# Performance work log

Measured on AMD Instinct MI355X. Metric: run time of the kernel, lower is better.

The kernel has to match this reference:

```python
import jax, jax.numpy as jnp
import numpy as np

DIM = 512
HEADS = 16
WIN = (7, 7)
N = WIN[0] * WIN[1]
B_ = 4096
HEAD_DIM = DIM // HEADS
SCALE = HEAD_DIM ** (-0.5)


def _relative_position_index():
    ch = np.arange(WIN[0])
    cw = np.arange(WIN[1])
    coords = np.stack(np.meshgrid(ch, cw, indexing='ij'))  # (2, Wh, Ww)
    cf = coords.reshape(2, -1)                               # (2, N)
    rel = cf[:, :, None] - cf[:, None, :]                    # (2, N, N)
    rel = rel.transpose(1, 2, 0).astype(np.int32)            # (N, N, 2)
    rel[:, :, 0] += WIN[0] - 1
    rel[:, :, 1] += WIN[1] - 1
    rel[:, :, 0] *= 2 * WIN[1] - 1
    return jnp.asarray(rel.sum(-1))                          # (N, N) int32


def setup_inputs() -> dict:
    key = jax.random.key(0)
    ks = jax.random.split(key, 6)
    x = jax.random.normal(ks[0], (B_, N, DIM), dtype=jnp.float32)
    qkv_w = jax.random.normal(ks[1], (3 * DIM, DIM), dtype=jnp.float32) * (DIM ** -0.5)
    qkv_b = jnp.zeros((3 * DIM,), dtype=jnp.float32)
    proj_w = jax.random.normal(ks[2], (DIM, DIM), dtype=jnp.float32) * (DIM ** -0.5)
    proj_b = jnp.zeros((DIM,), dtype=jnp.float32)
    n_rel = (2 * WIN[0] - 1) * (2 * WIN[1] - 1)  # 169
    bias_table = jax.random.normal(ks[3], (n_rel, HEADS), dtype=jnp.float32) * 0.02
    rel_idx = _relative_position_index()
    return {"x": x, "qkv_w": qkv_w, "qkv_b": qkv_b, "proj_w": proj_w,
            "proj_b": proj_b, "bias_table": bias_table, "rel_idx": rel_idx}


def reference(x, qkv_w, qkv_b, proj_w, proj_b, bias_table, rel_idx):
    B, n, C = x.shape
    # qkv projection: (B, N, 3C) -> (3, B, H, N, hd)
    qkv = x @ qkv_w.T + qkv_b
    qkv = qkv.reshape(B, n, 3, HEADS, HEAD_DIM).transpose(2, 0, 3, 1, 4)
    q, k, v = qkv[0], qkv[1], qkv[2]
    q = q * SCALE
    attn = jnp.einsum('bhnd,bhmd->bhnm', q, k)               # (B, H, N, N)
    # gather relative position bias: (N*N, H) -> (H, N, N)
    bias = bias_table[rel_idx.reshape(-1)].reshape(n, n, HEADS).transpose(2, 0, 1)
    attn = jax.nn.softmax(attn + bias[None], axis=-1)
    out = jnp.einsum('bhnm,bhmd->bhnd', attn, v)
    out = out.transpose(0, 2, 1, 3).reshape(B, n, C)
    return out @ proj_w.T + proj_b
```

## Files before the change

### kernel.cpp

```cpp
#include <hip/hip_runtime.h>
#include <cstdint>
#include <type_traits>

#define B_WIN 4096
#define NTOK 49
#define DIMC 512
#define HEADS 16
#define HD 32
#define M_ROWS (B_WIN * NTOK)
#define SCALE 0.17677669529663689f

using bf16x8 = __attribute__((ext_vector_type(8))) short;
using f32x4  = __attribute__((ext_vector_type(4))) float;
using u16x8  = __attribute__((ext_vector_type(8))) unsigned short;

__device__ inline unsigned short f2bf(float f) {
    uint32_t u = __float_as_uint(f);
    uint32_t r = (u + 0x7fffu + ((u >> 16) & 1u)) >> 16;
    return (unsigned short)r;
}
__device__ inline unsigned int pk2(float lo, float hi) {
    return (unsigned int)f2bf(lo) | ((unsigned int)f2bf(hi) << 16);
}

__device__ __forceinline__ void gll16(const unsigned short* g, unsigned short* l) {
    __builtin_amdgcn_global_load_lds(
        (const __attribute__((address_space(1))) void*)g,
        (__attribute__((address_space(3))) void*)l, 16, 0, 0);
}

#define DSR(dst, addr) asm volatile("ds_read_b128 %0, %1" : "=v"(dst) : "v"(addr))
#define SCHED0() __builtin_amdgcn_sched_barrier(0)
#define BARRIER() do { SCHED0(); __builtin_amdgcn_s_barrier(); SCHED0(); } while (0)
#define LGKM0() do { asm volatile("s_waitcnt lgkmcnt(0)"); SCHED0(); } while (0)

__global__ __launch_bounds__(256) void cvt_f32_bf16(
    const float* __restrict__ in, unsigned short* __restrict__ out, int n4)
{
    for (int i = blockIdx.x * blockDim.x + threadIdx.x; i < n4;
         i += gridDim.x * blockDim.x) {
        float4 v = reinterpret_cast<const float4*>(in)[i];
        ushort4 o;
        o.x = f2bf(v.x); o.y = f2bf(v.y); o.z = f2bf(v.z); o.w = f2bf(v.w);
        reinterpret_cast<ushort4*>(out)[i] = o;
    }
}

__global__ __launch_bounds__(256) void build_bias(
    const float* __restrict__ btab, const int* __restrict__ ridx,
    float* __restrict__ biasPad)
{
    const int idx = blockIdx.x * 256 + threadIdx.x;
    const int h = idx >> 12, rem = idx & 4095;
    const int i = rem >> 6, j = rem & 63;
    float v = -1e30f;
    if (i < NTOK && j < NTOK) v = btab[ridx[i * NTOK + j] * HEADS + h];
    biasPad[idx] = v;
}

template <int OUTF32>
__global__ __launch_bounds__(512, 2) void gemm8p(
    const unsigned short* __restrict__ A,
    const unsigned short* __restrict__ W,
    const float* __restrict__ bias,
    void* __restrict__ Craw,
    int N, int ntn)
{
    extern __shared__ unsigned short lds[];
    constexpr int K = 512, NT = 8;

    const int nwg = gridDim.x;
    const int bid = blockIdx.x;
    const int wg = (bid & 7) * (nwg >> 3) + (bid >> 3);
    const int tn = wg % ntn, tm = wg / ntn;
    const size_t m0 = (size_t)tm * 256, n0 = (size_t)tn * 256;

    const int t = threadIdx.x;
    const int lane = t & 63, wid = t >> 6;
    const int wm = wid >> 2, wn = wid & 3;
    const int l15 = lane & 15, l4 = lane >> 4;

    const unsigned short* pA[2];
    const unsigned short* pB[2];
    int dA[2], dB[2];
#pragma unroll
    for (int u = 0; u < 2; ++u) {
        const int f = t + u * 512, rl = f >> 3, c = f & 7, g = c ^ (rl & 7);
        const int lrA = (rl & 63) + (rl >> 6) * 128;
        const int lrB = ((rl >> 5) << 6) + (rl & 31);
        pA[u] = A + (m0 + lrA) * K + g * 8;
        pB[u] = W + (n0 + lrB) * K + g * 8;
        dA[u] = lrA * 64 + c * 8;
        dB[u] = 32768 + lrB * 64 + c * 8;
    }
#define STG_A(h, T) { const int _b = ((T) & 1) * 16384, _kt = (T) * 64;      \
    gll16(pA[0] + (h) * 64 * K + _kt, lds + _b + dA[0] + (h) * 4096);        \
    gll16(pA[1] + (h) * 64 * K + _kt, lds + _b + dA[1] + (h) * 4096); }
#define STG_B(h, T) { const int _b = ((T) & 1) * 16384, _kt = (T) * 64;      \
    gll16(pB[0] + (h) * 32 * K + _kt, lds + _b + dB[0] + (h) * 2048);        \
    gll16(pB[1] + (h) * 32 * K + _kt, lds + _b + dB[1] + (h) * 2048); }

    const unsigned lbase = (unsigned)(uintptr_t)lds;
    const unsigned swz = (unsigned)(l15 & 7);
    const unsigned cx0 = ((0u + l4) ^ swz) * 16u;
    const unsigned cx1 = ((4u + l4) ^ swz) * 16u;
    const unsigned arow = (unsigned)(wm * 128 + l15) * 128u;
    const unsigned brow = (unsigned)(wn * 64 + l15) * 128u;

    f32x4 acc[8][4] = {};
    bf16x8 a[4][2], b0[2][2], b1[2][2];

    STG_A(0, 0); STG_B(0, 0); STG_A(1, 0); STG_B(1, 0);
    STG_A(0, 1); STG_B(0, 1); STG_A(1, 1);
    asm volatile("s_waitcnt vmcnt(6)");
    SCHED0();
    BARRIER();

    for (int S = 0; S < NT; ++S) {
        const int bs = S & 1;
        const unsigned ab = lbase + (unsigned)bs * 32768u;
        const unsigned bb = lbase + 65536u + (unsigned)bs * 32768u;

#pragma unroll
        for (int m = 0; m < 4; ++m) {
            DSR(a[m][0], ab + arow + m * 2048u + cx0);
            DSR(a[m][1], ab + arow + m * 2048u + cx1);
        }
#pragma unroll
        for (int n = 0; n < 2; ++n) {
            DSR(b0[n][0], bb + brow + n * 2048u + cx0);
            DSR(b0[n][1], bb + brow + n * 2048u + cx1);
        }
        if (S + 1 < NT) STG_B(1, S + 1);
        BARRIER(); LGKM0();
        __builtin_amdgcn_s_setprio(1);
#pragma unroll
        for (int m = 0; m < 4; ++m)
#pragma unroll
            for (int n = 0; n < 2; ++n)
#pragma unroll
                for (int ks = 0; ks < 2; ++ks)
                    acc[m][n] = __builtin_amdgcn_mfma_f32_16x16x32_bf16(
                        a[m][ks], b0[n][ks], acc[m][n], 0, 0, 0);
        __builtin_amdgcn_s_setprio(0);
        BARRIER();

#pragma unroll
        for (int n = 0; n < 2; ++n) {
            DSR(b1[n][0], bb + brow + (n + 2) * 2048u + cx0);
            DSR(b1[n][1], bb + brow + (n + 2) * 2048u + cx1);
        }
        if (S + 2 < NT) STG_A(0, S + 2);
        BARRIER(); LGKM0();
        __builtin_amdgcn_s_setprio(1);
#pragma unroll
        for (int m = 0; m < 4; ++m)
#pragma unroll
            for (int n = 0; n < 2; ++n)
#pragma unroll
                for (int ks = 0; ks < 2; ++ks)
                    acc[m][n + 2] = __builtin_amdgcn_mfma_f32_16x16x32_bf16(
                        a[m][ks], b1[n][ks], acc[m][n + 2], 0, 0, 0);
        __builtin_amdgcn_s_setprio(0);
        BARRIER();

#pragma unroll
        for (int m = 0; m < 4; ++m) {
            DSR(a[m][0], ab + arow + 8192u + m * 2048u + cx0);
            DSR(a[m][1], ab + arow + 8192u + m * 2048u + cx1);
        }
        if (S + 2 < NT) STG_B(0, S + 2);
        BARRIER(); LGKM0();
        __builtin_amdgcn_s_setprio(1);
#pragma unroll
        for (int m = 0; m < 4; ++m)
#pragma unroll
            for (int n = 0; n < 2; ++n)
#pragma unroll
                for (int ks = 0; ks < 2; ++ks)
                    acc[m + 4][n] = __builtin_amdgcn_mfma_f32_16x16x32_bf16(
                        a[m][ks], b0[n][ks], acc[m + 4][n], 0, 0, 0);
        __builtin_amdgcn_s_setprio(0);
        BARRIER();

        if (S + 2 < NT) STG_A(1, S + 2);
        if (S < NT - 2)       { asm volatile("s_waitcnt vmcnt(6)"); SCHED0(); }
        else if (S == NT - 2) { asm volatile("s_waitcnt vmcnt(0)"); SCHED0(); }
        BARRIER();
        __builtin_amdgcn_s_setprio(1);
#pragma unroll
        for (int m = 0; m < 4; ++m)
#pragma unroll
            for (int n = 0; n < 2; ++n)
#pragma unroll
                for (int ks = 0; ks < 2; ++ks)
                    acc[m + 4][n + 2] = __builtin_amdgcn_mfma_f32_16x16x32_bf16(
                        a[m][ks], b1[n][ks], acc[m + 4][n + 2], 0, 0, 0);
        __builtin_amdgcn_s_setprio(0);
        BARRIER();
    }

#pragma unroll
    for (int m = 0; m < 8; ++m) {
#pragma unroll
        for (int n = 0; n < 4; ++n) {
            const size_t col = n0 + wn * 64 + n * 16 + l15;
            const float bv = bias[col];
#pragma unroll
            for (int r = 0; r < 4; ++r) {
                const size_t row = m0 + wm * 128 + m * 16 + l4 * 4 + r;
                const float v = acc[m][n][r] + bv;
                if constexpr (OUTF32)
                    ((float*)Craw)[row * N + col] = v;
                else
                    ((unsigned short*)Craw)[row * N + col] = f2bf(v);
            }
        }
    }
#undef STG_A
#undef STG_B
}

__global__ __launch_bounds__(256) void attn_mfma(
    const unsigned short* __restrict__ qkv,
    const float* __restrict__ biasPad,
    unsigned short* __restrict__ attn_out)
{
    __shared__ unsigned short vtile[4][32][72];

    const int w = threadIdx.x >> 6;
    const int g = blockIdx.x * 4 + w;
    const int b = g >> 4, h = g & 15;
    const int lane = threadIdx.x & 63;
    const int l15 = lane & 15, l4 = lane >> 4;

    bf16x8 aq[4], bk[4], vload[4];
#pragma unroll
    for (int mt = 0; mt < 4; ++mt) {
        const int tok = mt * 16 + l15;
        bf16x8 zq = {}, zk = {}, zv = {};
        if (tok < NTOK) {
            const unsigned short* base =
                qkv + (size_t)(b * NTOK + tok) * 1536 + h * HD + l4 * 8;
            zq = *(const bf16x8*)base;
            zk = *(const bf16x8*)(base + 512);
            zv = *(const bf16x8*)(base + 1024);
        }
        aq[mt] = zq; bk[mt] = zk; vload[mt] = zv;
    }

#pragma unroll
    for (int mt = 0; mt < 4; ++mt) {
        const int tok = mt * 16 + l15;
#pragma unroll
        for (int e = 0; e < 8; ++e)
            vtile[w][l4 * 8 + e][tok] = (unsigned short)vload[mt][e];
    }

    f32x4 sacc[4][4] = {};
#pragma unroll
    for (int nt = 0; nt < 4; ++nt)
#pragma unroll
        for (int mt = 0; mt < 4; ++mt)
            sacc[nt][mt] = __builtin_amdgcn_mfma_f32_16x16x32_bf16(
                bk[nt], aq[mt], sacc[nt][mt], 0, 0, 0);

    const float* bb = biasPad + (h << 12);
    unsigned int pw[4][4][2];
#pragma unroll
    for (int mt = 0; mt < 4; ++mt) {
        const int i = mt * 16 + l15;
        const float* brow = bb + i * 64 + l4 * 4;
        float mx = -3.0e38f;
#pragma unroll
        for (int nt = 0; nt < 4; ++nt) {
            const float4 b4 = *(const float4*)(brow + nt * 16);
            const float v0 = fmaf(sacc[nt][mt][0], SCALE, b4.x);
            const float v1 = fmaf(sacc[nt][mt][1], SCALE, b4.y);
            const float v2 = fmaf(sacc[nt][mt][2], SCALE, b4.z);
            const float v3 = fmaf(sacc[nt][mt][3], SCALE, b4.w);
            sacc[nt][mt][0] = v0; sacc[nt][mt][1] = v1;
            sacc[nt][mt][2] = v2; sacc[nt][mt][3] = v3;
            mx = fmaxf(mx, fmaxf(fmaxf(v0, v1), fmaxf(v2, v3)));
        }
        mx = fmaxf(mx, __shfl_xor(mx, 16));
        mx = fmaxf(mx, __shfl_xor(mx, 32));
        float sum = 0.f;
#pragma unroll
        for (int nt = 0; nt < 4; ++nt) {
            const float e0 = __expf(sacc[nt][mt][0] - mx);
            const float e1 = __expf(sacc[nt][mt][1] - mx);
            const float e2 = __expf(sacc[nt][mt][2] - mx);
            const float e3 = __expf(sacc[nt][mt][3] - mx);
            sacc[nt][mt][0] = e0; sacc[nt][mt][1] = e1;
            sacc[nt][mt][2] = e2; sacc[nt][mt][3] = e3;
            sum += (e0 + e1) + (e2 + e3);
        }
        sum += __shfl_xor(sum, 16);
        sum += __shfl_xor(sum, 32);
        const float inv = 1.0f / sum;
#pragma unroll
        for (int nt = 0; nt < 4; ++nt) {
            pw[mt][nt][0] = pk2(sacc[nt][mt][0] * inv, sacc[nt][mt][1] * inv);
            pw[mt][nt][1] = pk2(sacc[nt][mt][2] * inv, sacc[nt][mt][3] * inv);
        }
    }

    bf16x8 ap[4][2];
#pragma unroll
    for (int mt = 0; mt < 4; ++mt)
#pragma unroll
        for (int ks = 0; ks < 2; ++ks) {
            union { int wv[4]; bf16x8 v; } u;
#pragma unroll
            for (int q = 0; q < 4; ++q) {
                const int src = l15 + ((2 * (l4 & 1) + (q >> 1)) << 4);
                const int va = __shfl((int)pw[mt][2 * ks][q & 1], src);
                const int vb = __shfl((int)pw[mt][2 * ks + 1][q & 1], src);
                u.wv[q] = (l4 & 2) ? vb : va;
            }
            ap[mt][ks] = u.v;
        }

    bf16x8 bv2[2][2];
#pragma unroll
    for (int n = 0; n < 2; ++n)
#pragma unroll
        for (int ks = 0; ks < 2; ++ks)
            bv2[n][ks] = *(const bf16x8*)&vtile[w][n * 16 + l15][ks * 32 + l4 * 8];

    f32x4 oacc[4][2] = {};
#pragma unroll
    for (int mt = 0; mt < 4; ++mt)
#pragma unroll
        for (int n = 0; n < 2; ++n)
#pragma unroll
            for (int ks = 0; ks < 2; ++ks)
                oacc[mt][n] = __builtin_amdgcn_mfma_f32_16x16x32_bf16(
                    ap[mt][ks], bv2[n][ks], oacc[mt][n], 0, 0, 0);

#pragma unroll
    for (int mt = 0; mt < 4; ++mt) {
#pragma unroll
        for (int r = 0; r < 4; ++r) {
            const int i = mt * 16 + l4 * 4 + r;
            if (i < NTOK) {
                unsigned short* op =
                    attn_out + (size_t)(b * NTOK + i) * DIMC + h * HD + l15;
                op[0]  = f2bf(oacc[mt][0][r]);
                op[16] = f2bf(oacc[mt][1][r]);
            }
        }
    }
}

extern "C" void kernel_launch(void* const* d_in, const int* in_sizes, int n_in,
                              void* d_out, int out_size, void* d_ws, size_t ws_size,
                              hipStream_t stream)
{
    const float* x      = (const float*)d_in[0];
    const float* qkv_w  = (const float*)d_in[1];
    const float* qkv_b  = (const float*)d_in[2];
    const float* proj_w = (const float*)d_in[3];
    const float* proj_b = (const float*)d_in[4];
    const float* btab   = (const float*)d_in[5];
    const int*   ridx   = (const int*)d_in[6];
    float* out = (float*)d_out;

    char* w = (char*)d_ws;
    const size_t SZ_XBF   = (size_t)M_ROWS * DIMC * 2;
    const size_t SZ_QKVW  = (size_t)1536 * 512 * 2;
    const size_t SZ_PROJW = (size_t)512 * 512 * 2;
    const size_t SZ_BIAS  = (size_t)HEADS * 64 * 64 * 4;
    const size_t SZ_QKV   = (size_t)M_ROWS * 1536 * 2;
    unsigned short* x_bf     = (unsigned short*)w;
    unsigned short* qkvw_bf  = (unsigned short*)(w + SZ_XBF);
    unsigned short* projw_bf = (unsigned short*)(w + SZ_XBF + SZ_QKVW);
    float*          biasPad  = (float*)(w + SZ_XBF + SZ_QKVW + SZ_PROJW);
    unsigned short* qkv      = (unsigned short*)(w + SZ_XBF + SZ_QKVW + SZ_PROJW + SZ_BIAS);
    unsigned short* attn_out = (unsigned short*)((char*)qkv + SZ_QKV);

    hipFuncSetAttribute(reinterpret_cast<const void*>(&gemm8p<0>),
                        hipFuncAttributeMaxDynamicSharedMemorySize, 131072);
    hipFuncSetAttribute(reinterpret_cast<const void*>(&gemm8p<1>),
                        hipFuncAttributeMaxDynamicSharedMemorySize, 131072);

    cvt_f32_bf16<<<2048, 256, 0, stream>>>(x, x_bf, M_ROWS * DIMC / 4);
    cvt_f32_bf16<<<128, 256, 0, stream>>>(qkv_w, qkvw_bf, 1536 * 512 / 4);
    cvt_f32_bf16<<<64, 256, 0, stream>>>(proj_w, projw_bf, 512 * 512 / 4);
    build_bias<<<256, 256, 0, stream>>>(btab, ridx, biasPad);

    gemm8p<0><<<4704, 512, 131072, stream>>>(
        x_bf, qkvw_bf, qkv_b, qkv, 1536, 6);

    attn_mfma<<<16384, 256, 0, stream>>>(qkv, biasPad, attn_out);

    gemm8p<1><<<1568, 512, 131072, stream>>>(
        attn_out, projw_bf, proj_b, out, 512, 2);
}
```

Before: 938.9 us.

## Fuse x fp32-to-bf16 conversion into QKV GEMM A-tile loading

Removes the separate conversion kernel for x and has the QKV GEMM load fp32 A tiles through registers, convert them to bf16 and write them to LDS inside its pipeline. This avoids writing and re-reading a bf16 copy of x. In exchange, A loads no longer use direct global-to-LDS transfers, which adds register pressure, conversion ALU work and extra wait points in the pipelined loop. The GEMM also reads twice as many A bytes per tile.

New measurement: 1.022 ms. +8.9%, slower.

```diff
diff --git a/kernel.cpp b/kernel.cpp
--- a/kernel.cpp
+++ b/kernel.cpp
@@ -33,6 +33,7 @@
 #define SCHED0() __builtin_amdgcn_sched_barrier(0)
 #define BARRIER() do { SCHED0(); __builtin_amdgcn_s_barrier(); SCHED0(); } while (0)
 #define LGKM0() do { asm volatile("s_waitcnt lgkmcnt(0)"); SCHED0(); } while (0)
+#define VMCNT(n) do { asm volatile("s_waitcnt vmcnt(" #n ")"); SCHED0(); } while (0)
 
 __global__ __launch_bounds__(256) void cvt_f32_bf16(
     const float* __restrict__ in, unsigned short* __restrict__ out, int n4)
@@ -58,9 +59,9 @@
     biasPad[idx] = v;
 }
 
-template <int OUTF32>
+template <int AF32, int OUTF32>
 __global__ __launch_bounds__(512, 2) void gemm8p(
-    const unsigned short* __restrict__ A,
+    const void* __restrict__ Araw,
     const unsigned short* __restrict__ W,
     const float* __restrict__ bias,
     void* __restrict__ Craw,
@@ -81,6 +82,7 @@
     const int l15 = lane & 15, l4 = lane >> 4;
 
     const unsigned short* pA[2];
+    const float* fA[2];
     const unsigned short* pB[2];
     int dA[2], dB[2];
 #pragma unroll
@@ -88,7 +90,10 @@
         const int f = t + u * 512, rl = f >> 3, c = f & 7, g = c ^ (rl & 7);
         const int lrA = (rl & 63) + (rl >> 6) * 128;
         const int lrB = ((rl >> 5) << 6) + (rl & 31);
-        pA[u] = A + (m0 + lrA) * K + g * 8;
+        if constexpr (AF32)
+            fA[u] = (const float*)Araw + (m0 + lrA) * K + g * 8;
+        else
+            pA[u] = (const unsigned short*)Araw + (m0 + lrA) * K + g * 8;
         pB[u] = W + (n0 + lrB) * K + g * 8;
         dA[u] = lrA * 64 + c * 8;
         dB[u] = 32768 + lrB * 64 + c * 8;
@@ -99,6 +104,18 @@
 #define STG_B(h, T) { const int _b = ((T) & 1) * 16384, _kt = (T) * 64;      \
     gll16(pB[0] + (h) * 32 * K + _kt, lds + _b + dB[0] + (h) * 2048);        \
     gll16(pB[1] + (h) * 32 * K + _kt, lds + _b + dB[1] + (h) * 2048); }
+#define LDA_H(dst, h, T) { const int _kt = (T) * 64 + (h) * 32768;           \
+    dst[0] = *(const float4*)(fA[0] + _kt);                                  \
+    dst[1] = *(const float4*)(fA[0] + _kt + 4);                              \
+    dst[2] = *(const float4*)(fA[1] + _kt);                                  \
+    dst[3] = *(const float4*)(fA[1] + _kt + 4); }
+#define WRA_H(s, h, T) { const int _b = ((T) & 1) * 16384; u16x8 _w0, _w1;   \
+    _w0[0]=f2bf(s[0].x); _w0[1]=f2bf(s[0].y); _w0[2]=f2bf(s[0].z); _w0[3]=f2bf(s[0].w); \
+    _w0[4]=f2bf(s[1].x); _w0[5]=f2bf(s[1].y); _w0[6]=f2bf(s[1].z); _w0[7]=f2bf(s[1].w); \
+    _w1[0]=f2bf(s[2].x); _w1[1]=f2bf(s[2].y); _w1[2]=f2bf(s[2].z); _w1[3]=f2bf(s[2].w); \
+    _w1[4]=f2bf(s[3].x); _w1[5]=f2bf(s[3].y); _w1[6]=f2bf(s[3].z); _w1[7]=f2bf(s[3].w); \
+    *(u16x8*)(lds + _b + dA[0] + (h) * 4096) = _w0;                          \
+    *(u16x8*)(lds + _b + dA[1] + (h) * 4096) = _w1; }
 
     const unsigned lbase = (unsigned)(uintptr_t)lds;
     const unsigned swz = (unsigned)(l15 & 7);
@@ -109,12 +126,28 @@
 
     f32x4 acc[8][4] = {};
     bf16x8 a[4][2], b0[2][2], b1[2][2];
-
-    STG_A(0, 0); STG_B(0, 0); STG_A(1, 0); STG_B(1, 0);
-    STG_A(0, 1); STG_B(0, 1); STG_A(1, 1);
-    asm volatile("s_waitcnt vmcnt(6)");
-    SCHED0();
-    BARRIER();
+    float4 a0l[4], a1l[4];
+
+    if constexpr (AF32) {
+        LDA_H(a0l, 0, 0); LDA_H(a1l, 1, 0);
+        SCHED0();
+        STG_B(0, 0); STG_B(1, 0);
+        VMCNT(4);
+        WRA_H(a0l, 0, 0); WRA_H(a1l, 1, 0);
+        SCHED0();
+        LDA_H(a0l, 0, 1); LDA_H(a1l, 1, 1);
+        SCHED0();
+        STG_B(0, 1);
+        VMCNT(2);
+        WRA_H(a0l, 0, 1); WRA_H(a1l, 1, 1);
+        LGKM0();
+        BARRIER();
+    } else {
+        STG_A(0, 0); STG_B(0, 0); STG_A(1, 0); STG_B(1, 0);
+        STG_A(0, 1); STG_B(0, 1); STG_A(1, 1);
+        VMCNT(6);
+        BARRIER();
+    }
 
     for (int S = 0; S < NT; ++S) {
         const int bs = S & 1;
@@ -131,6 +164,10 @@
             DSR(b0[n][0], bb + brow + n * 2048u + cx0);
             DSR(b0[n][1], bb + brow + n * 2048u + cx1);
         }
+        SCHED0();
+        if constexpr (AF32) {
+            if (S + 2 < NT) { LDA_H(a0l, 0, S + 2); SCHED0(); }
+        }
         if (S + 1 < NT) STG_B(1, S + 1);
         BARRIER(); LGKM0();
         __builtin_amdgcn_s_setprio(1);
@@ -150,7 +187,18 @@
             DSR(b1[n][0], bb + brow + (n + 2) * 2048u + cx0);
             DSR(b1[n][1], bb + brow + (n + 2) * 2048u + cx1);
         }
-        if (S + 2 < NT) STG_A(0, S + 2);
+        SCHED0();
+        if constexpr (AF32) {
+            if (S + 2 < NT) {
+                LDA_H(a1l, 1, S + 2);
+                SCHED0();
+                VMCNT(6);
+                WRA_H(a0l, 0, S + 2);
+                SCHED0();
+            }
+        } else {
+            if (S + 2 < NT) STG_A(0, S + 2);
+        }
         BARRIER(); LGKM0();
         __builtin_amdgcn_s_setprio(1);
 #pragma unroll
@@ -169,6 +217,7 @@
             DSR(a[m][0], ab + arow + 8192u + m * 2048u + cx0);
             DSR(a[m][1], ab + arow + 8192u + m * 2048u + cx1);
         }
+        SCHED0();
         if (S + 2 < NT) STG_B(0, S + 2);
         BARRIER(); LGKM0();
         __builtin_amdgcn_s_setprio(1);
@@ -183,9 +232,17 @@
         __builtin_amdgcn_s_setprio(0);
         BARRIER();
 
-        if (S + 2 < NT) STG_A(1, S + 2);
-        if (S < NT - 2)       { asm volatile("s_waitcnt vmcnt(6)"); SCHED0(); }
-        else if (S == NT - 2) { asm volatile("s_waitcnt vmcnt(0)"); SCHED0(); }
+        if constexpr (AF32) {
+            if (S + 2 < NT) {
+                VMCNT(2);
+                WRA_H(a1l, 1, S + 2);
+                SCHED0();
+            } else if (S == NT - 2) { VMCNT(0); }
+        } else {
+            if (S + 2 < NT) STG_A(1, S + 2);
+            if (S < NT - 2)       { VMCNT(6); }
+            else if (S == NT - 2) { VMCNT(0); }
+        }
         BARRIER();
         __builtin_amdgcn_s_setprio(1);
 #pragma unroll
@@ -219,6 +276,8 @@
     }
 #undef STG_A
 #undef STG_B
+#undef LDA_H
+#undef WRA_H
 }
 
 __global__ __launch_bounds__(256) void attn_mfma(
@@ -368,33 +427,30 @@
     float* out = (float*)d_out;
 
     char* w = (char*)d_ws;
-    const size_t SZ_XBF   = (size_t)M_ROWS * DIMC * 2;
     const size_t SZ_QKVW  = (size_t)1536 * 512 * 2;
     const size_t SZ_PROJW = (size_t)512 * 512 * 2;
     const size_t SZ_BIAS  = (size_t)HEADS * 64 * 64 * 4;
     const size_t SZ_QKV   = (size_t)M_ROWS * 1536 * 2;
-    unsigned short* x_bf     = (unsigned short*)w;
-    unsigned short* qkvw_bf  = (unsigned short*)(w + SZ_XBF);
-    unsigned short* projw_bf = (unsigned short*)(w + SZ_XBF + SZ_QKVW);
-    float*          biasPad  = (float*)(w + SZ_XBF + SZ_QKVW + SZ_PROJW);
-    unsigned short* qkv      = (unsigned short*)(w + SZ_XBF + SZ_QKVW + SZ_PROJW + SZ_BIAS);
+    unsigned short* qkvw_bf  = (unsigned short*)w;
+    unsigned short* projw_bf = (unsigned short*)(w + SZ_QKVW);
+    float*          biasPad  = (float*)(w + SZ_QKVW + SZ_PROJW);
+    unsigned short* qkv      = (unsigned short*)(w + SZ_QKVW + SZ_PROJW + SZ_BIAS);
     unsigned short* attn_out = (unsigned short*)((char*)qkv + SZ_QKV);
 
-    hipFuncSetAttribute(reinterpret_cast<const void*>(&gemm8p<0>),
+    hipFuncSetAttribute(reinterpret_cast<const void*>(&gemm8p<1, 0>),
                         hipFuncAttributeMaxDynamicSharedMemorySize, 131072);
-    hipFuncSetAttribute(reinterpret_cast<const void*>(&gemm8p<1>),
+    hipFuncSetAttribute(reinterpret_cast<const void*>(&gemm8p<0, 1>),
                         hipFuncAttributeMaxDynamicSharedMemorySize, 131072);
 
-    cvt_f32_bf16<<<2048, 256, 0, stream>>>(x, x_bf, M_ROWS * DIMC / 4);
     cvt_f32_bf16<<<128, 256, 0, stream>>>(qkv_w, qkvw_bf, 1536 * 512 / 4);
     cvt_f32_bf16<<<64, 256, 0, stream>>>(proj_w, projw_bf, 512 * 512 / 4);
     build_bias<<<256, 256, 0, stream>>>(btab, ridx, biasPad);
 
-    gemm8p<0><<<4704, 512, 131072, stream>>>(
-        x_bf, qkvw_bf, qkv_b, qkv, 1536, 6);
+    gemm8p<1, 0><<<4704, 512, 131072, stream>>>(
+        x, qkvw_bf, qkv_b, qkv, 1536, 6);
 
     attn_mfma<<<16384, 256, 0, stream>>>(qkv, biasPad, attn_out);
 
-    gemm8p<1><<<1568, 512, 131072, stream>>>(
+    gemm8p<0, 1><<<1568, 512, 131072, stream>>>(
         attn_out, projw_bf, proj_b, out, 512, 2);
 }
```

## Compute two adjacent N tiles per GEMM workgroup with continuous pipelined K loop

Applied to the files above, without the earlier changes.

Each GEMM workgroup now covers two 256-wide N tiles. It runs one continuous software-pipelined loop over 16 K-steps and writes the epilogue for the first tile midway through. The A tile is reloaded from global memory (likely from L2), but the pipeline prologue and drain happen once per two tiles and the grid is half as large. The trade-off is fewer workgroups, which can hurt load balance, and a mid-loop epilogue of stores that may stall the pipeline.

New measurement: 1.628 ms. +73.4%, slower.

```diff
diff --git a/kernel.cpp b/kernel.cpp
--- a/kernel.cpp
+++ b/kernel.cpp
@@ -33,6 +33,7 @@
 #define SCHED0() __builtin_amdgcn_sched_barrier(0)
 #define BARRIER() do { SCHED0(); __builtin_amdgcn_s_barrier(); SCHED0(); } while (0)
 #define LGKM0() do { asm volatile("s_waitcnt lgkmcnt(0)"); SCHED0(); } while (0)
+#define VMCNT(n) do { asm volatile("s_waitcnt vmcnt(" #n ")"); SCHED0(); } while (0)
 
 __global__ __launch_bounds__(256) void cvt_f32_bf16(
     const float* __restrict__ in, unsigned short* __restrict__ out, int n4)
@@ -58,7 +59,7 @@
     biasPad[idx] = v;
 }
 
-template <int OUTF32>
+template <int NPASS, int OUTF32>
 __global__ __launch_bounds__(512, 2) void gemm8p(
     const unsigned short* __restrict__ A,
     const unsigned short* __restrict__ W,
@@ -67,13 +68,14 @@
     int N, int ntn)
 {
     extern __shared__ unsigned short lds[];
-    constexpr int K = 512, NT = 8;
+    constexpr int K = 512;
+    constexpr int NTT = 8 * NPASS;
 
     const int nwg = gridDim.x;
     const int bid = blockIdx.x;
     const int wg = (bid & 7) * (nwg >> 3) + (bid >> 3);
     const int tn = wg % ntn, tm = wg / ntn;
-    const size_t m0 = (size_t)tm * 256, n0 = (size_t)tn * 256;
+    const size_t m0 = (size_t)tm * 256, n0 = (size_t)tn * (256 * NPASS);
 
     const int t = threadIdx.x;
     const int lane = t & 63, wid = t >> 6;
@@ -93,12 +95,13 @@
         dA[u] = lrA * 64 + c * 8;
         dB[u] = 32768 + lrB * 64 + c * 8;
     }
-#define STG_A(h, T) { const int _b = ((T) & 1) * 16384, _kt = (T) * 64;      \
+#define STG_A(h, T) { const int _b = ((T) & 1) * 16384, _kt = ((T) & 7) * 64; \
     gll16(pA[0] + (h) * 64 * K + _kt, lds + _b + dA[0] + (h) * 4096);        \
     gll16(pA[1] + (h) * 64 * K + _kt, lds + _b + dA[1] + (h) * 4096); }
-#define STG_B(h, T) { const int _b = ((T) & 1) * 16384, _kt = (T) * 64;      \
-    gll16(pB[0] + (h) * 32 * K + _kt, lds + _b + dB[0] + (h) * 2048);        \
-    gll16(pB[1] + (h) * 32 * K + _kt, lds + _b + dB[1] + (h) * 2048); }
+#define STG_B(h, T) { const int _b = ((T) & 1) * 16384;                      \
+    const size_t _ko = (size_t)((T) >> 3) * (256 * K) + ((T) & 7) * 64;      \
+    gll16(pB[0] + (h) * 32 * K + _ko, lds + _b + dB[0] + (h) * 2048);        \
+    gll16(pB[1] + (h) * 32 * K + _ko, lds + _b + dB[1] + (h) * 2048); }
 
     const unsigned lbase = (unsigned)(uintptr_t)lds;
     const unsigned swz = (unsigned)(l15 & 7);
@@ -107,16 +110,33 @@
     const unsigned arow = (unsigned)(wm * 128 + l15) * 128u;
     const unsigned brow = (unsigned)(wn * 64 + l15) * 128u;
 
+    float br0[4], br1[4];
+#pragma unroll
+    for (int n = 0; n < 4; ++n) {
+        br0[n] = bias[n0 + wn * 64 + n * 16 + l15];
+        br1[n] = (NPASS == 2) ? bias[n0 + 256 + wn * 64 + n * 16 + l15] : 0.0f;
+    }
+
     f32x4 acc[8][4] = {};
     bf16x8 a[4][2], b0[2][2], b1[2][2];
 
+#define EPI(p, BR) {                                                         \
+    _Pragma("unroll") for (int m = 0; m < 8; ++m) {                          \
+        _Pragma("unroll") for (int n = 0; n < 4; ++n) {                      \
+            const size_t col = n0 + (p) * 256 + wn * 64 + n * 16 + l15;      \
+            _Pragma("unroll") for (int r = 0; r < 4; ++r) {                  \
+                const size_t row = m0 + wm * 128 + m * 16 + l4 * 4 + r;      \
+                const float v = acc[m][n][r] + BR[n];                        \
+                if constexpr (OUTF32) ((float*)Craw)[row * N + col] = v;     \
+                else ((unsigned short*)Craw)[row * N + col] = f2bf(v);       \
+                acc[m][n][r] = 0.0f; } } } }
+
     STG_A(0, 0); STG_B(0, 0); STG_A(1, 0); STG_B(1, 0);
     STG_A(0, 1); STG_B(0, 1); STG_A(1, 1);
-    asm volatile("s_waitcnt vmcnt(6)");
-    SCHED0();
+    VMCNT(6);
     BARRIER();
 
-    for (int S = 0; S < NT; ++S) {
+    for (int S = 0; S < NTT; ++S) {
         const int bs = S & 1;
         const unsigned ab = lbase + (unsigned)bs * 32768u;
         const unsigned bb = lbase + 65536u + (unsigned)bs * 32768u;
@@ -131,7 +151,7 @@
             DSR(b0[n][0], bb + brow + n * 2048u + cx0);
             DSR(b0[n][1], bb + brow + n * 2048u + cx1);
         }
-        if (S + 1 < NT) STG_B(1, S + 1);
+        if (S + 1 < NTT) STG_B(1, S + 1);
         BARRIER(); LGKM0();
         __builtin_amdgcn_s_setprio(1);
 #pragma unroll
@@ -150,7 +170,7 @@
             DSR(b1[n][0], bb + brow + (n + 2) * 2048u + cx0);
             DSR(b1[n][1], bb + brow + (n + 2) * 2048u + cx1);
         }
-        if (S + 2 < NT) STG_A(0, S + 2);
+        if (S + 2 < NTT) STG_A(0, S + 2);
         BARRIER(); LGKM0();
         __builtin_amdgcn_s_setprio(1);
 #pragma unroll
@@ -169,7 +189,7 @@
             DSR(a[m][0], ab + arow + 8192u + m * 2048u + cx0);
             DSR(a[m][1], ab + arow + 8192u + m * 2048u + cx1);
         }
-        if (S + 2 < NT) STG_B(0, S + 2);
+        if (S + 2 < NTT) STG_B(0, S + 2);
         BARRIER(); LGKM0();
         __builtin_amdgcn_s_setprio(1);
 #pragma unroll
@@ -183,9 +203,9 @@
         __builtin_amdgcn_s_setprio(0);
         BARRIER();
 
-        if (S + 2 < NT) STG_A(1, S + 2);
-        if (S < NT - 2)       { asm volatile("s_waitcnt vmcnt(6)"); SCHED0(); }
-        else if (S == NT - 2) { asm volatile("s_waitcnt vmcnt(0)"); SCHED0(); }
+        if (S + 2 < NTT) STG_A(1, S + 2);
+        if (S < NTT - 2)       { VMCNT(6); }
+        else if (S == NTT - 2) { VMCNT(0); }
         BARRIER();
         __builtin_amdgcn_s_setprio(1);
 #pragma unroll
@@ -198,27 +218,15 @@
                         a[m][ks], b1[n][ks], acc[m + 4][n + 2], 0, 0, 0);
         __builtin_amdgcn_s_setprio(0);
         BARRIER();
-    }
-
-#pragma unroll
-    for (int m = 0; m < 8; ++m) {
-#pragma unroll
-        for (int n = 0; n < 4; ++n) {
-            const size_t col = n0 + wn * 64 + n * 16 + l15;
-            const float bv = bias[col];
-#pragma unroll
-            for (int r = 0; r < 4; ++r) {
-                const size_t row = m0 + wm * 128 + m * 16 + l4 * 4 + r;
-                const float v = acc[m][n][r] + bv;
-                if constexpr (OUTF32)
-                    ((float*)Craw)[row * N + col] = v;
-                else
-                    ((unsigned short*)Craw)[row * N + col] = f2bf(v);
-            }
+
+        if ((S & 7) == 7) {
+            if ((S >> 3) == 0) { EPI(0, br0); }
+            else               { EPI(1, br1); }
         }
     }
 #undef STG_A
 #undef STG_B
+#undef EPI
 }
 
 __global__ __launch_bounds__(256) void attn_mfma(
@@ -380,9 +388,9 @@
     unsigned short* qkv      = (unsigned short*)(w + SZ_XBF + SZ_QKVW + SZ_PROJW + SZ_BIAS);
     unsigned short* attn_out = (unsigned short*)((char*)qkv + SZ_QKV);
 
-    hipFuncSetAttribute(reinterpret_cast<const void*>(&gemm8p<0>),
+    hipFuncSetAttribute(reinterpret_cast<const void*>(&gemm8p<2, 0>),
                         hipFuncAttributeMaxDynamicSharedMemorySize, 131072);
-    hipFuncSetAttribute(reinterpret_cast<const void*>(&gemm8p<1>),
+    hipFuncSetAttribute(reinterpret_cast<const void*>(&gemm8p<2, 1>),
                         hipFuncAttributeMaxDynamicSharedMemorySize, 131072);
 
     cvt_f32_bf16<<<2048, 256, 0, stream>>>(x, x_bf, M_ROWS * DIMC / 4);
@@ -390,11 +398,11 @@
     cvt_f32_bf16<<<64, 256, 0, stream>>>(proj_w, projw_bf, 512 * 512 / 4);
     build_bias<<<256, 256, 0, stream>>>(btab, ridx, biasPad);
 
-    gemm8p<0><<<4704, 512, 131072, stream>>>(
-        x_bf, qkvw_bf, qkv_b, qkv, 1536, 6);
+    gemm8p<2, 0><<<2352, 512, 131072, stream>>>(
+        x_bf, qkvw_bf, qkv_b, qkv, 1536, 3);
 
     attn_mfma<<<16384, 256, 0, stream>>>(qkv, biasPad, attn_out);
 
-    gemm8p<1><<<1568, 512, 131072, stream>>>(
-        attn_out, projw_bf, proj_b, out, 512, 2);
-}
+    gemm8p<2, 1><<<784, 512, 131072, stream>>>(
+        attn_out, projw_bf, proj_b, out, 512, 1);
+}
```
